# Kernel optimization log

Measured on AMD Instinct MI355X. Metric: run time of the kernel, lower is better.

Reference implementation:

```python
import jax, jax.numpy as jnp
import numpy as np

N = 100000   # nodes
E = 1600000  # edges
D = 64       # in_channels
H = 64       # hidden_channels
G = 1000     # number of graphs (100 nodes each)


def _xavier(key, fan_in, fan_out):
    a = np.sqrt(6.0 / (fan_in + fan_out)).astype(np.float32)
    return jax.random.uniform(key, (fan_in, fan_out), jnp.float32, -a, a)


def setup_inputs() -> dict:
    key = jax.random.key(0)
    ks = jax.random.split(key, 6)
    x = jax.random.normal(ks[0], (N, D), jnp.float32)
    edge_index = jax.random.randint(ks[1], (2, E), 0, N, dtype=jnp.int32)
    edge_weight = jax.random.uniform(ks[2], (E,), jnp.float32)
    # every graph id 0..G-1 occurs exactly N//G times (sorted)
    batch = (jnp.arange(N, dtype=jnp.int32) // (N // G)).astype(jnp.int32)
    W1 = _xavier(ks[3], D, H); b1 = jnp.zeros((H,), jnp.float32)
    W2 = _xavier(ks[4], H, H); b2 = jnp.zeros((H,), jnp.float32)
    W3 = _xavier(ks[5], H, 1); b3 = jnp.zeros((1,), jnp.float32)
    return dict(x=x, edge_index=edge_index, edge_weight=edge_weight, batch=batch,
                W1=W1, b1=b1, W2=W2, b2=b2, W3=W3, b3=b3)


def reference(x, edge_index, edge_weight, batch, W1, b1, W2, b2, W3, b3):
    src, dst = edge_index[0], edge_index[1]
    # nodes per graph (torch.bincount(batch)) and broadcast back to nodes
    counts = jax.ops.segment_sum(jnp.ones((N,), jnp.float32), batch, num_segments=G)
    cpn = counts[batch]  # [N]

    def mpnn_layer(h, W, b):
        # gather x_j, scale by edge weight, scatter-add to target nodes
        m = h[src] * edge_weight[:, None]              # [E, C]
        agg = jax.ops.segment_sum(m, dst, num_segments=N)  # [N, C]
        out = agg / cpn[:, None]                       # per-node normalize
        return out @ W + b

    h = jax.nn.sigmoid(mpnn_layer(x, W1, b1))
    h = jax.nn.sigmoid(mpnn_layer(h, W2, b2))
    h = mpnn_layer(h, W3, b3)                          # [N, 1]
    # global mean pool over each graph
    pooled = jax.ops.segment_sum(h, batch, num_segments=G) / counts[:, None]
    return pooled  # [G, 1]
```

## Files before the change

### kernel.cpp

```cpp
#include <hip/hip_runtime.h>
#include <hip/hip_fp16.h>
#include <math.h>

#define NN 100000
#define EE 1600000
#define GG 1000
#define NPG 100
#define NBUK 391
#define BCAP 4608
#define EPB 8192
#define NBINBLK ((EE + EPB - 1) / EPB)
#define GEMM1BLK ((NN + 127) / 128)
#define GEMM2BLK ((NN + 63) / 64)

typedef __attribute__((ext_vector_type(8))) short short8v;
typedef __attribute__((ext_vector_type(4))) float float4v;

__device__ __forceinline__ unsigned char f32_to_fp8(float a) {
    return (unsigned char)(__builtin_amdgcn_cvt_pk_fp8_f32(a, a, 0, false) & 0xFF);
}
__device__ __forceinline__ float fp8_to_f32(unsigned b) {
    return __builtin_amdgcn_cvt_f32_fp8((int)b, 0);
}
__device__ __forceinline__ unsigned short f32_to_bf16(float f) {
    unsigned u = __float_as_uint(f);
    unsigned r = u + 0x7FFFu + ((u >> 16) & 1u);
    return (unsigned short)(r >> 16);
}

#if __has_builtin(__builtin_amdgcn_cvt_pk_f32_fp8)
typedef float floatx2 __attribute__((ext_vector_type(2)));
#define HAVE_PK_CVT 1
#else
#define HAVE_PK_CVT 0
#endif

__device__ __forceinline__ void unpack4(unsigned dw, float* f) {
#if HAVE_PK_CVT
    floatx2 lo = __builtin_amdgcn_cvt_pk_f32_fp8(dw, false);
    floatx2 hi = __builtin_amdgcn_cvt_pk_f32_fp8(dw, true);
    f[0] = lo.x; f[1] = lo.y; f[2] = hi.x; f[3] = hi.y;
#else
    f[0] = fp8_to_f32(dw & 0xFF);
    f[1] = fp8_to_f32((dw >> 8) & 0xFF);
    f[2] = fp8_to_f32((dw >> 16) & 0xFF);
    f[3] = fp8_to_f32((dw >> 24) & 0xFF);
#endif
}

__device__ __forceinline__ float4v mfma16(short8v a, short8v b, float4v c) {
    return __builtin_amdgcn_mfma_f32_16x16x32_bf16(a, b, c, 0, 0, 0);
}
__device__ __forceinline__ short8v fp8x8_to_bf16frag(uint2 q) {
    float f[8];
    unpack4(q.x, f);
    unpack4(q.y, f + 4);
    short8v s;
#pragma unroll
    for (int j = 0; j < 8; j++) s[j] = (short)f32_to_bf16(f[j]);
    return s;
}
__device__ __forceinline__ short8v f32x8_to_bf16frag(float4 a, float4 b) {
    short8v s;
    s[0] = (short)f32_to_bf16(a.x); s[1] = (short)f32_to_bf16(a.y);
    s[2] = (short)f32_to_bf16(a.z); s[3] = (short)f32_to_bf16(a.w);
    s[4] = (short)f32_to_bf16(b.x); s[5] = (short)f32_to_bf16(b.y);
    s[6] = (short)f32_to_bf16(b.z); s[7] = (short)f32_to_bf16(b.w);
    return s;
}
template<int NT>
__device__ __forceinline__ void stageW(const float* __restrict__ W,
                                       unsigned short* Wt, int tid) {
    for (int i = tid; i < 4096; i += NT) {
        int k = i >> 6, c = i & 63;
        Wt[(c << 6) | (((k >> 3) ^ (c & 7)) << 3) | (k & 7)] = f32_to_bf16(W[i]);
    }
}
__device__ __forceinline__ short8v ldB(const unsigned short* Wt, int col, int g) {
    return *(const short8v*)&Wt[(col << 6) | ((g ^ (col & 7)) << 3)];
}
__device__ __forceinline__ void mfma_tile_store(short8v a_lo, short8v a_hi,
                                                const unsigned short* Wt,
                                                int row0, int lane,
                                                unsigned char* __restrict__ out, int n) {
    int rl = lane & 15, kg = lane >> 4;
#pragma unroll
    for (int ct = 0; ct < 4; ct++) {
        int col = ct * 16 + rl;
        short8v blo = ldB(Wt, col, kg);
        short8v bhi = ldB(Wt, col, 4 + kg);
        float4v acc = {0.f, 0.f, 0.f, 0.f};
        acc = mfma16(a_lo, blo, acc);
        acc = mfma16(a_hi, bhi, acc);
        int dr = (lane >> 4) * 4;
#pragma unroll
        for (int r = 0; r < 4; r++) {
            int R = row0 + dr + r;
            if (R < n) out[(size_t)R * 64 + col] = f32_to_fp8(acc[r]);
        }
    }
}

__global__ __launch_bounds__(512)
void k_binbound(const int* __restrict__ src, const int* __restrict__ dst,
                const float* __restrict__ ew, int* __restrict__ bukcnt,
                uint2* __restrict__ ep1, int* __restrict__ rowptr, int E) {
    __shared__ int hist[NBUK];
    __shared__ int gbase[NBUK];
    int tid = threadIdx.x;
    if (blockIdx.x == 0 && tid == 0) rowptr[NN] = EE;
    for (int i = tid; i < NBUK; i += 512) hist[i] = 0;
    __syncthreads();
    int base = blockIdx.x * EPB;
    int b[16], rank[16];
    unsigned x[16], w[16];
#pragma unroll
    for (int u = 0; u < 16; u++) {
        int e = base + u * 512 + tid;
        if (e < E) {
            int d = dst[e];
            b[u] = d >> 8;
            x[u] = ((unsigned)(d & 255) << 24) | (unsigned)src[e];
            w[u] = __float_as_uint(ew[e]);
            rank[u] = atomicAdd(&hist[b[u]], 1);
        } else b[u] = -1;
    }
    __syncthreads();
    for (int i = tid; i < NBUK; i += 512) {
        int h = hist[i];
        gbase[i] = h ? atomicAdd(&bukcnt[i], h) : 0;
    }
    __syncthreads();
#pragma unroll
    for (int u = 0; u < 16; u++) {
        if (b[u] >= 0) ep1[(size_t)b[u] * BCAP + gbase[b[u]] + rank[u]] = make_uint2(x[u], w[u]);
    }
}

__global__ __launch_bounds__(512)
void k_bin2gemm1(const uint2* __restrict__ ep1, const int* __restrict__ bukcnt,
                 unsigned* __restrict__ ep2, int* __restrict__ rowptr,
                 const float* __restrict__ x, const float* __restrict__ W1,
                 unsigned char* __restrict__ t, int n) {
    __shared__ __align__(16) unsigned char smem[41984];
    int tid = threadIdx.x;
    int bk = blockIdx.x;
    if (bk < NBUK) {
        uint2* stage = (uint2*)smem;
        int* h   = (int*)(smem + 36864);
        int* s   = h + 256;
        int* cur = s + 256;
        int* sc  = cur + 256;
        int v = (tid < NBUK) ? bukcnt[tid] : 0;
        sc[tid] = v;
        __syncthreads();
        for (int off = 1; off < 512; off <<= 1) {
            int tv = (tid >= off) ? sc[tid - off] : 0;
            __syncthreads();
            sc[tid] += tv;
            __syncthreads();
        }
        int cnt = bukcnt[bk];
        int base = sc[bk] - cnt;
        if (tid < 256) h[tid] = 0;
        __syncthreads();
        size_t ebase = (size_t)bk * BCAP;
        for (int e = tid; e < cnt; e += 512) {
            uint2 r = ep1[ebase + e];
            stage[e] = r;
            atomicAdd(&h[r.x >> 24], 1);
        }
        __syncthreads();
        if (tid < 256) s[tid] = h[tid];
        __syncthreads();
        for (int off = 1; off < 256; off <<= 1) {
            int tv = 0;
            if (tid < 256 && tid >= off) tv = s[tid - off];
            __syncthreads();
            if (tid < 256) s[tid] += tv;
            __syncthreads();
        }
        if (tid < 256) {
            int pfx = base + s[tid] - h[tid];
            int node = bk * 256 + tid;
            if (node < n) rowptr[node] = pfx;
            cur[tid] = pfx;
        }
        __syncthreads();
        for (int e = tid; e < cnt; e += 512) {
            uint2 r = stage[e];
            int pos = atomicAdd(&cur[r.x >> 24], 1);
            unsigned wq = (unsigned)fminf(__uint_as_float(r.y) * 32768.f + 0.5f, 32767.f);
            ep2[pos] = (wq << 17) | (r.x & 0x1FFFFu);
        }
    } else {
        unsigned short* Wt = (unsigned short*)smem;
        stageW<512>(W1, Wt, tid);
        __syncthreads();
        int w = tid >> 6, lane = tid & 63;
        int row0 = (bk - NBUK) * 128 + w * 16;
        int rl = lane & 15, kg = lane >> 4;
        int rsrc = row0 + rl;
        if (rsrc > n - 1) rsrc = n - 1;
        const float* ar = x + (size_t)rsrc * 64 + kg * 8;
        float4 f0 = *(const float4*)ar;
        float4 f1 = *(const float4*)(ar + 4);
        float4 f2 = *(const float4*)(ar + 32);
        float4 f3 = *(const float4*)(ar + 36);
        short8v a_lo = f32x8_to_bf16frag(f0, f1);
        short8v a_hi = f32x8_to_bf16frag(f2, f3);
        mfma_tile_store(a_lo, a_hi, Wt, row0, lane, t, n);
    }
}

__global__ __launch_bounds__(256)
void k_gemm64_mfma(const unsigned char* __restrict__ inp, const float* __restrict__ W,
                   unsigned char* __restrict__ out, int n) {
    __shared__ __align__(16) unsigned short Wt[64 * 64];
    int tid = threadIdx.x;
    stageW<256>(W, Wt, tid);
    __syncthreads();
    int w = tid >> 6, lane = tid & 63;
    int row0 = blockIdx.x * 64 + w * 16;
    int rl = lane & 15, kg = lane >> 4;
    int rsrc = row0 + rl;
    if (rsrc > n - 1) rsrc = n - 1;
    const unsigned char* ar = inp + (size_t)rsrc * 64 + kg * 8;
    uint2 qlo = *(const uint2*)ar;
    uint2 qhi = *(const uint2*)(ar + 32);
    short8v a_lo = fp8x8_to_bf16frag(qlo);
    short8v a_hi = fp8x8_to_bf16frag(qhi);
    mfma_tile_store(a_lo, a_hi, Wt, row0, lane, out, n);
}

template<int MODE>
__global__ __launch_bounds__(256)
void k_gather64(const unsigned char* __restrict__ t, const int* __restrict__ rowptr,
                const unsigned* __restrict__ ep, void* __restrict__ outp,
                const float* __restrict__ bv, const float* __restrict__ W3,
                int n) {
    int wid = (blockIdx.x * blockDim.x + threadIdx.x) >> 6;
    int lane = threadIdx.x & 63;
    wid = __builtin_amdgcn_readfirstlane(wid);
    if (wid >= n) return;
    int beg = rowptr[wid], end = rowptr[wid + 1];
    int q = lane >> 4;
    unsigned sl4 = (unsigned)(lane & 15) * 4u;
    float ax = 0.f, ay = 0.f, az = 0.f, aw = 0.f;
    for (int base = beg; base < end; base += 64) {
        int el = base + lane;
        unsigned wl = 0u;
        if (el < end) wl = ep[el];
        int nE = end - base; if (nE > 64) nE = 64;
        int ng = (nE + 3) >> 2;
        for (int g0 = 0; g0 < ng; g0 += 4) {
            unsigned vv[4];
            float wt[4];
#pragma unroll
            for (int p = 0; p < 4; p++) {
                unsigned wq = __shfl(wl, (g0 + p) * 4 + q, 64);
                wt[p] = (float)(wq >> 17);
                vv[p] = *(const unsigned*)(t + ((wq & 0x1FFFFu) * 64u + sl4));
            }
#pragma unroll
            for (int p = 0; p < 4; p++) {
                float f[4];
                unpack4(vv[p], f);
                ax = fmaf(wt[p], f[0], ax);
                ay = fmaf(wt[p], f[1], ay);
                az = fmaf(wt[p], f[2], az);
                aw = fmaf(wt[p], f[3], aw);
            }
        }
    }
    ax += __shfl_xor(ax, 16, 64); ax += __shfl_xor(ax, 32, 64);
    ay += __shfl_xor(ay, 16, 64); ay += __shfl_xor(ay, 32, 64);
    az += __shfl_xor(az, 16, 64); az += __shfl_xor(az, 32, 64);
    aw += __shfl_xor(aw, 16, 64); aw += __shfl_xor(aw, 32, 64);

    const float Cn = 0x1p-15f / (float)NPG;
    float4 bb = ((const float4*)bv)[lane & 15];
    float v0 = ax * Cn + bb.x, v1 = ay * Cn + bb.y;
    float v2 = az * Cn + bb.z, v3 = aw * Cn + bb.w;
    v0 = 1.f / (1.f + __expf(-v0));
    v1 = 1.f / (1.f + __expf(-v1));
    v2 = 1.f / (1.f + __expf(-v2));
    v3 = 1.f / (1.f + __expf(-v3));
    if (MODE == 0) {
        if (q == 0) {
            unsigned r = (unsigned)__builtin_amdgcn_cvt_pk_fp8_f32(v0, v1, 0, false);
            r = (unsigned)__builtin_amdgcn_cvt_pk_fp8_f32(v2, v3, (int)r, true);
            ((unsigned*)outp)[(size_t)wid * 16 + (lane & 15)] = r;
        }
    } else {
        float4 w4 = ((const float4*)W3)[lane & 15];
        float d = v0 * w4.x + v1 * w4.y + v2 * w4.z + v3 * w4.w;
        d += __shfl_xor(d, 1, 64);
        d += __shfl_xor(d, 2, 64);
        d += __shfl_xor(d, 4, 64);
        d += __shfl_xor(d, 8, 64);
        if (lane == 0) ((float*)outp)[wid] = d;
    }
}

__global__ __launch_bounds__(256)
void k_y3pool(const float* __restrict__ y, const int* __restrict__ rowptr,
              const unsigned* __restrict__ ep,
              const float* __restrict__ b3, float* __restrict__ out) {
    __shared__ float red[256];
    int g = blockIdx.x;
    int tid = threadIdx.x;
    int ebeg = rowptr[g * NPG], eend = rowptr[g * NPG + NPG];
    float acc = 0.f;
    for (int e = ebeg + tid; e < eend; e += 256) {
        unsigned r = ep[e];
        unsigned off = (r & 0x1FFFFu) * 4u;
        acc = fmaf((float)(r >> 17), *(const float*)((const char*)y + off), acc);
    }
    red[tid] = acc;
    __syncthreads();
    for (int off = 128; off > 0; off >>= 1) {
        if (tid < off) red[tid] += red[tid + off];
        __syncthreads();
    }
    if (tid == 0) {
        out[g] = red[0] * 0x1p-15f / ((float)NPG * (float)NPG) + b3[0];
    }
}

extern "C" void kernel_launch(void* const* d_in, const int* in_sizes, int n_in,
                              void* d_out, int out_size, void* d_ws, size_t ws_size,
                              hipStream_t stream) {
    const float* x     = (const float*)d_in[0];
    const int*   ei    = (const int*)d_in[1];
    const int*   src   = ei;
    const int*   dst   = ei + EE;
    const float* ew    = (const float*)d_in[2];
    const float* W1    = (const float*)d_in[4];
    const float* b1    = (const float*)d_in[5];
    const float* W2    = (const float*)d_in[6];
    const float* b2    = (const float*)d_in[7];
    const float* W3    = (const float*)d_in[8];
    const float* b3    = (const float*)d_in[9];
    float* out = (float*)d_out;

    unsigned char* t   = (unsigned char*)d_ws;
    unsigned char* t2  = t + (size_t)NN * 64;
    unsigned char* hh8 = t2 + (size_t)NN * 64;
    float* y      = (float*)(hh8 + (size_t)NN * 64);
    unsigned* ep2 = (unsigned*)(y + NN);
    int*   bukcnt = (int*)(ep2 + EE);
    int*   rowptr = bukcnt + NBUK + 1;
    uint2* ep1    = (uint2*)(rowptr + NN + 2);

    hipMemsetAsync(bukcnt, 0, NBUK * sizeof(int), stream);

    k_binbound<<<NBINBLK, 512, 0, stream>>>(src, dst, ew, bukcnt, ep1, rowptr, EE);

    k_bin2gemm1<<<NBUK + GEMM1BLK, 512, 0, stream>>>(ep1, bukcnt, ep2, rowptr, x, W1, t, NN);

    int gblk = (int)(((size_t)NN * 64 + 255) / 256);

    k_gather64<0><<<gblk, 256, 0, stream>>>(t, rowptr, ep2, hh8, b1, nullptr, NN);

    k_gemm64_mfma<<<GEMM2BLK, 256, 0, stream>>>(hh8, W2, t2, NN);

    k_gather64<1><<<gblk, 256, 0, stream>>>(t2, rowptr, ep2, y, b2, W3, NN);

    k_y3pool<<<GG, 256, 0, stream>>>(y, rowptr, ep2, b3, out);
}
```

Baseline: 214.1 us.

## Process four nodes per wavefront in gather with batched up-front loads

Each wavefront in the gather kernel now handles four destination nodes. It loads all four edge lists and issues up to 32 feature gathers per node before any accumulation, so many independent memory loads are in flight at once. Edges beyond 32 per node go through a scalar-strided tail loop. This targets memory latency and per-node loop overhead, in exchange for more registers per thread, lower occupancy, and relying on NN being divisible by four.

```diff
diff --git a/kernel.cpp b/kernel.cpp
--- a/kernel.cpp
+++ b/kernel.cpp
@@ -238,68 +238,106 @@
 void k_gather64(const unsigned char* __restrict__ t, const int* __restrict__ rowptr,
                 const unsigned* __restrict__ ep, void* __restrict__ outp,
                 const float* __restrict__ bv, const float* __restrict__ W3,
-                int n) {
+                int nq) {
     int wid = (blockIdx.x * blockDim.x + threadIdx.x) >> 6;
     int lane = threadIdx.x & 63;
     wid = __builtin_amdgcn_readfirstlane(wid);
-    if (wid >= n) return;
-    int beg = rowptr[wid], end = rowptr[wid + 1];
+    if (wid >= nq) return;
+    int n0 = wid * 4;
     int q = lane >> 4;
     unsigned sl4 = (unsigned)(lane & 15) * 4u;
-    float ax = 0.f, ay = 0.f, az = 0.f, aw = 0.f;
-    for (int base = beg; base < end; base += 64) {
-        int el = base + lane;
-        unsigned wl = 0u;
-        if (el < end) wl = ep[el];
-        int nE = end - base; if (nE > 64) nE = 64;
-        int ng = (nE + 3) >> 2;
-        for (int g0 = 0; g0 < ng; g0 += 4) {
-            unsigned vv[4];
-            float wt[4];
-#pragma unroll
-            for (int p = 0; p < 4; p++) {
-                unsigned wq = __shfl(wl, (g0 + p) * 4 + q, 64);
-                wt[p] = (float)(wq >> 17);
-                vv[p] = *(const unsigned*)(t + ((wq & 0x1FFFFu) * 64u + sl4));
+
+    int rp[5];
+#pragma unroll
+    for (int i = 0; i < 5; i++) rp[i] = rowptr[n0 + i];
+
+    unsigned wl[4];
+#pragma unroll
+    for (int i = 0; i < 4; i++) {
+        int e = rp[i] + lane;
+        wl[i] = (e < rp[i + 1]) ? ep[e] : 0u;
+    }
+
+    unsigned vA[4][4];
+#pragma unroll
+    for (int i = 0; i < 4; i++) {
+#pragma unroll
+        for (int g = 0; g < 4; g++) {
+            unsigned wq = __shfl(wl[i], g * 4 + q, 64);
+            vA[i][g] = *(const unsigned*)(t + ((wq & 0x1FFFFu) * 64u + sl4));
+        }
+    }
+    unsigned vB[4][4];
+#pragma unroll
+    for (int i = 0; i < 4; i++) {
+        if (rp[i + 1] - rp[i] > 16) {
+#pragma unroll
+            for (int g = 0; g < 4; g++) {
+                unsigned wq = __shfl(wl[i], 16 + g * 4 + q, 64);
+                vB[i][g] = *(const unsigned*)(t + ((wq & 0x1FFFFu) * 64u + sl4));
             }
-#pragma unroll
-            for (int p = 0; p < 4; p++) {
-                float f[4];
-                unpack4(vv[p], f);
-                ax = fmaf(wt[p], f[0], ax);
-                ay = fmaf(wt[p], f[1], ay);
-                az = fmaf(wt[p], f[2], az);
-                aw = fmaf(wt[p], f[3], aw);
-            }
-        }
-    }
-    ax += __shfl_xor(ax, 16, 64); ax += __shfl_xor(ax, 32, 64);
-    ay += __shfl_xor(ay, 16, 64); ay += __shfl_xor(ay, 32, 64);
-    az += __shfl_xor(az, 16, 64); az += __shfl_xor(az, 32, 64);
-    aw += __shfl_xor(aw, 16, 64); aw += __shfl_xor(aw, 32, 64);
+        }
+    }
 
     const float Cn = 0x1p-15f / (float)NPG;
     float4 bb = ((const float4*)bv)[lane & 15];
-    float v0 = ax * Cn + bb.x, v1 = ay * Cn + bb.y;
-    float v2 = az * Cn + bb.z, v3 = aw * Cn + bb.w;
-    v0 = 1.f / (1.f + __expf(-v0));
-    v1 = 1.f / (1.f + __expf(-v1));
-    v2 = 1.f / (1.f + __expf(-v2));
-    v3 = 1.f / (1.f + __expf(-v3));
-    if (MODE == 0) {
-        if (q == 0) {
-            unsigned r = (unsigned)__builtin_amdgcn_cvt_pk_fp8_f32(v0, v1, 0, false);
-            r = (unsigned)__builtin_amdgcn_cvt_pk_fp8_f32(v2, v3, (int)r, true);
-            ((unsigned*)outp)[(size_t)wid * 16 + (lane & 15)] = r;
-        }
-    } else {
-        float4 w4 = ((const float4*)W3)[lane & 15];
-        float d = v0 * w4.x + v1 * w4.y + v2 * w4.z + v3 * w4.w;
-        d += __shfl_xor(d, 1, 64);
-        d += __shfl_xor(d, 2, 64);
-        d += __shfl_xor(d, 4, 64);
-        d += __shfl_xor(d, 8, 64);
-        if (lane == 0) ((float*)outp)[wid] = d;
+    float4 w4 = (MODE == 1) ? ((const float4*)W3)[lane & 15] : make_float4(0, 0, 0, 0);
+
+#pragma unroll
+    for (int i = 0; i < 4; i++) {
+        float ax = 0.f, ay = 0.f, az = 0.f, aw = 0.f;
+#pragma unroll
+        for (int g = 0; g < 4; g++) {
+            unsigned wq = __shfl(wl[i], g * 4 + q, 64);
+            float wt = (float)(wq >> 17);
+            float f[4];
+            unpack4(vA[i][g], f);
+            ax = fmaf(wt, f[0], ax); ay = fmaf(wt, f[1], ay);
+            az = fmaf(wt, f[2], az); aw = fmaf(wt, f[3], aw);
+        }
+        if (rp[i + 1] - rp[i] > 16) {
+#pragma unroll
+            for (int g = 0; g < 4; g++) {
+                unsigned wq = __shfl(wl[i], 16 + g * 4 + q, 64);
+                float wt = (float)(wq >> 17);
+                float f[4];
+                unpack4(vB[i][g], f);
+                ax = fmaf(wt, f[0], ax); ay = fmaf(wt, f[1], ay);
+                az = fmaf(wt, f[2], az); aw = fmaf(wt, f[3], aw);
+            }
+        }
+        for (int e = rp[i] + 32 + q; e < rp[i + 1]; e += 4) {
+            unsigned wq = ep[e];
+            float wt = (float)(wq >> 17);
+            float f[4];
+            unpack4(*(const unsigned*)(t + ((wq & 0x1FFFFu) * 64u + sl4)), f);
+            ax = fmaf(wt, f[0], ax); ay = fmaf(wt, f[1], ay);
+            az = fmaf(wt, f[2], az); aw = fmaf(wt, f[3], aw);
+        }
+        ax += __shfl_xor(ax, 16, 64); ax += __shfl_xor(ax, 32, 64);
+        ay += __shfl_xor(ay, 16, 64); ay += __shfl_xor(ay, 32, 64);
+        az += __shfl_xor(az, 16, 64); az += __shfl_xor(az, 32, 64);
+        aw += __shfl_xor(aw, 16, 64); aw += __shfl_xor(aw, 32, 64);
+        float v0 = ax * Cn + bb.x, v1 = ay * Cn + bb.y;
+        float v2 = az * Cn + bb.z, v3 = aw * Cn + bb.w;
+        v0 = 1.f / (1.f + __expf(-v0));
+        v1 = 1.f / (1.f + __expf(-v1));
+        v2 = 1.f / (1.f + __expf(-v2));
+        v3 = 1.f / (1.f + __expf(-v3));
+        if (MODE == 0) {
+            if (q == 0) {
+                unsigned r = (unsigned)__builtin_amdgcn_cvt_pk_fp8_f32(v0, v1, 0, false);
+                r = (unsigned)__builtin_amdgcn_cvt_pk_fp8_f32(v2, v3, (int)r, true);
+                ((unsigned*)outp)[(size_t)(n0 + i) * 16 + (lane & 15)] = r;
+            }
+        } else {
+            float d = v0 * w4.x + v1 * w4.y + v2 * w4.z + v3 * w4.w;
+            d += __shfl_xor(d, 1, 64);
+            d += __shfl_xor(d, 2, 64);
+            d += __shfl_xor(d, 4, 64);
+            d += __shfl_xor(d, 8, 64);
+            if (lane == 0) ((float*)outp)[n0 + i] = d;
+        }
     }
 }
 
@@ -359,13 +397,14 @@
 
     k_bin2gemm1<<<NBUK + GEMM1BLK, 512, 0, stream>>>(ep1, bukcnt, ep2, rowptr, x, W1, t, NN);
 
-    int gblk = (int)(((size_t)NN * 64 + 255) / 256);
-
-    k_gather64<0><<<gblk, 256, 0, stream>>>(t, rowptr, ep2, hh8, b1, nullptr, NN);
+    int nq = NN / 4;
+    int gblk = (nq * 64 + 255) / 256;
+
+    k_gather64<0><<<gblk, 256, 0, stream>>>(t, rowptr, ep2, hh8, b1, nullptr, nq);
 
     k_gemm64_mfma<<<GEMM2BLK, 256, 0, stream>>>(hh8, W2, t2, NN);
 
-    k_gather64<1><<<gblk, 256, 0, stream>>>(t2, rowptr, ep2, y, b2, W3, NN);
+    k_gather64<1><<<gblk, 256, 0, stream>>>(t2, rowptr, ep2, y, b2, W3, nq);
 
     k_y3pool<<<GG, 256, 0, stream>>>(y, rowptr, ep2, b3, out);
 }
```

Result: faster. 204.8 us (-4.3%).
